# Performance work log

Measured on AMD Instinct MI355X. Metric: run time of the kernel, lower is better.

Reference implementation:

```python
import jax, jax.numpy as jnp
import numpy as np

EPSILON = 100.0
NITER = 10


def setup_inputs() -> dict:
    key = jax.random.key(0)
    k1, k2 = jax.random.split(key)
    n, d = 1024, 256
    output = jax.random.normal(k1, (n, d), dtype=jnp.float32)
    target = jax.random.normal(k2, (n, d), dtype=jnp.float32)
    return {"output": output, "target": target}


def _sinkhorn_loss_primal(x, y, epsilon, niter):
    n = x.shape[0]
    # L1 pairwise cost: C[i, j] = sum_k |x[i, k] - y[j, k]|   -> [n, n]
    C = jnp.sum(jnp.abs(x[:, None, :] - y[None, :, :]), axis=-1)
    log_mu = jnp.log(jnp.full((n,), 1.0 / n, dtype=x.dtype))
    log_nu = log_mu

    def M(u, v):
        # (-c_ij + u_i + v_j) / epsilon
        return (-C + u[:, None] + v[None, :]) / epsilon

    def lse_rows(A):
        # matches torch: log(sum(exp(A), axis=1) + 1e-6) (unstabilized on purpose)
        return jnp.log(jnp.sum(jnp.exp(A), axis=1) + 1e-6)

    def body(carry, _):
        u, v, done = carry
        u_new = epsilon * (log_mu - lse_rows(M(u, v))) + u
        v_new = epsilon * (log_nu - lse_rows(M(u_new, v).T)) + v
        err = jnp.sum(jnp.abs(u_new - u))
        # early exit emulation: once err < 0.1 after a step, freeze duals
        u_out = jnp.where(done, u, u_new)
        v_out = jnp.where(done, v, v_new)
        done_out = jnp.logical_or(done, err < 0.1)
        return (u_out, v_out, done_out), None

    u0 = jnp.zeros((n,), dtype=x.dtype)
    v0 = jnp.zeros((n,), dtype=x.dtype)
    (u, v, _), _ = jax.lax.scan(body, (u0, v0, jnp.array(False)), None, length=niter)

    Gamma = jnp.exp(M(u, v))
    return jnp.sum(Gamma * C)


def reference(output, target):
    # normalized=False path of FeatureOptimalLoss.forward
    return _sinkhorn_loss_primal(output, target, EPSILON, NITER)
```

## Files before the change

kernel.cpp:

```cpp
#include <hip/hip_runtime.h>
#include <stdint.h>

#define N 1024
#define DD 256
#define EPS 100.0f
#define INV_EPS 0.01f
#define LOG_MU -6.93147180559945f

__device__ __forceinline__ float waveReduceSum(float s) {
#pragma unroll
  for (int m = 1; m <= 32; m <<= 1) s += __shfl_xor(s, m);
  return s;
}

__device__ __forceinline__ uint64_t rload64(const uint64_t* p) {
  return __hip_atomic_load(p, __ATOMIC_RELAXED, __HIP_MEMORY_SCOPE_AGENT);
}
__device__ __forceinline__ void rstore64(uint64_t* p, uint64_t x) {
  __hip_atomic_store(p, x, __ATOMIC_RELAXED, __HIP_MEMORY_SCOPE_AGENT);
}
__device__ __forceinline__ uint64_t packtag(uint32_t tag, float val) {
  return ((uint64_t)tag << 32) | (uint64_t)__float_as_uint(val);
}

__device__ __forceinline__ void stage_exp(const uint64_t* __restrict__ src,
                                          uint32_t want, float* sB, int t) {
  const int base = t * 4;
  for (;;) {
    const uint64_t a0 = rload64(src + base + 0);
    const uint64_t a1 = rload64(src + base + 1);
    const uint64_t a2 = rload64(src + base + 2);
    const uint64_t a3 = rload64(src + base + 3);
    if ((uint32_t)(a0 >> 32) == want && (uint32_t)(a1 >> 32) == want &&
        (uint32_t)(a2 >> 32) == want && (uint32_t)(a3 >> 32) == want) {
      sB[base + 0] = expf(__uint_as_float((uint32_t)a0) * INV_EPS);
      sB[base + 1] = expf(__uint_as_float((uint32_t)a1) * INV_EPS);
      sB[base + 2] = expf(__uint_as_float((uint32_t)a2) * INV_EPS);
      sB[base + 3] = expf(__uint_as_float((uint32_t)a3) * INV_EPS);
      return;
    }
    __builtin_amdgcn_s_sleep(1);
  }
}

#define NTAGS 6160

__global__ __launch_bounds__(256) void cmat_kernel(
    const float* __restrict__ x, const float* __restrict__ y,
    float* __restrict__ Km, float* __restrict__ KTm,
    uint64_t* __restrict__ tags) {
  __shared__ float xs[64][68];
  __shared__ float ys[32][68];
  const int t = threadIdx.x;
  const int bj = blockIdx.x;
  const int bi = blockIdx.y;
  if (bi == 0 && bj == 0) {
    for (int z = t; z < NTAGS; z += 256) tags[z] = 0;
  }
  const int tx = t & 15;
  const int ty = t >> 4;
  float acc[4][2] = {};
  const float* xg = x + (size_t)(bi * 64) * DD;
  const float* yg = y + (size_t)(bj * 32) * DD;
  const int c0 = tx * 2, c1 = tx * 2 + 1;
  const int yswz = ((c0 >> 3) & 1) << 2;

  for (int kc = 0; kc < DD; kc += 64) {
    __syncthreads();
#pragma unroll
    for (int it = 0; it < 4; ++it) {
      const int l = it * 256 + t;
      const int row = l >> 4, kq = l & 15;
      const float4 g =
          *reinterpret_cast<const float4*>(xg + row * DD + kc + kq * 4);
      *reinterpret_cast<float4*>(&xs[row][kq * 4]) = g;
    }
#pragma unroll
    for (int it = 0; it < 2; ++it) {
      const int l = it * 256 + t;
      const int row = l >> 4, kq = l & 15;
      const float4 g =
          *reinterpret_cast<const float4*>(yg + row * DD + kc + kq * 4);
      const int col = (kq * 4) ^ (((row >> 3) & 1) << 2);
      *reinterpret_cast<float4*>(&ys[row][col]) = g;
    }
    __syncthreads();
#pragma unroll 2
    for (int kk = 0; kk < 64; kk += 4) {
      float4 xr[4];
#pragma unroll
      for (int r = 0; r < 4; ++r)
        xr[r] = *reinterpret_cast<const float4*>(&xs[ty * 4 + r][kk]);
      const float4 ya = *reinterpret_cast<const float4*>(&ys[c0][kk ^ yswz]);
      const float4 yb = *reinterpret_cast<const float4*>(&ys[c1][kk ^ yswz]);
#pragma unroll
      for (int r = 0; r < 4; ++r) {
        acc[r][0] += fabsf(xr[r].x - ya.x) + fabsf(xr[r].y - ya.y) +
                     fabsf(xr[r].z - ya.z) + fabsf(xr[r].w - ya.w);
        acc[r][1] += fabsf(xr[r].x - yb.x) + fabsf(xr[r].y - yb.y) +
                     fabsf(xr[r].z - yb.z) + fabsf(xr[r].w - yb.w);
      }
    }
  }
  float kv[4][2];
#pragma unroll
  for (int r = 0; r < 4; ++r) {
    kv[r][0] = expf(-acc[r][0] * INV_EPS);
    kv[r][1] = expf(-acc[r][1] * INV_EPS);
  }
  const int gr0 = bi * 64 + ty * 4;
  const int gc0 = bj * 32 + c0;
#pragma unroll
  for (int r = 0; r < 4; ++r)
    *reinterpret_cast<float2*>(Km + (size_t)(gr0 + r) * N + gc0) =
        make_float2(kv[r][0], kv[r][1]);
  __syncthreads();
#pragma unroll
  for (int r = 0; r < 4; ++r) {
    xs[c0][ty * 4 + r] = kv[r][0];
    xs[c1][ty * 4 + r] = kv[r][1];
  }
  __syncthreads();
#pragma unroll
  for (int it = 0; it < 2; ++it) {
    const int l = it * 256 + t;
    const int crow = l >> 4, cq = l & 15;
    const float4 val = *reinterpret_cast<const float4*>(&xs[crow][cq * 4]);
    *reinterpret_cast<float4*>(KTm + (size_t)(bj * 32 + crow) * N + bi * 64 +
                               cq * 4) = val;
  }
}

__global__ __launch_bounds__(256, 1) void sinkhorn_coop(
    const float* __restrict__ Km, const float* __restrict__ KTm,
    uint64_t* __restrict__ U, uint64_t* __restrict__ V,
    uint64_t* __restrict__ DERR, uint64_t* __restrict__ PART,
    uint64_t* __restrict__ DONE, float* __restrict__ out) {
  const int b = blockIdx.x, t = threadIdx.x;
  const int lane = t & 63, w = t >> 6;

  if (b == 256) {
    if (w != 0) return;
    for (int it = 0; it < 9; ++it) {
      const uint32_t k = it + 1;
      float e = 0.f;
#pragma unroll
      for (int q = 0; q < 16; ++q) {
        const int idx = q * 64 + lane;
        uint64_t d;
        while ((uint32_t)((d = rload64(DERR + idx)) >> 32) != k)
          __builtin_amdgcn_s_sleep(1);
        e += __uint_as_float((uint32_t)d);
      }
      e = waveReduceSum(e);
      if (lane == 0)
        rstore64(DONE + it, ((uint64_t)k << 32) | (e < 0.1f ? 1u : 0u));
      if (__shfl(e, 0) < 0.1f) return;
    }
    return;
  }

  __shared__ float sB[N];
  __shared__ float sRed[4];
  __shared__ int sDone;
  const int i = b * 4 + w;
  const float* Krow = Km + (size_t)i * N;
  const float* Trow = KTm + (size_t)i * N;

  float ui = 0.f, vj = 0.f;
  int klast = 0;

  for (int it = 0; it < 10; ++it) {
    const uint32_t k = it + 1;
    if (it == 0) {
      *reinterpret_cast<float4*>(&sB[t * 4]) = make_float4(1.f, 1.f, 1.f, 1.f);
    } else {
      stage_exp(V + (size_t)((k - 1) & 1) * N, k - 1, sB, t);
    }
    __syncthreads();
    {
      float s = 0.f;
#pragma unroll
      for (int q = 0; q < 4; ++q) {
        const int j4 = (q * 64 + lane) * 4;
        const float4 k4 = *reinterpret_cast<const float4*>(Krow + j4);
        s += k4.x * sB[j4] + k4.y * sB[j4 + 1] + k4.z * sB[j4 + 2] +
             k4.w * sB[j4 + 3];
      }
      s = waveReduceSum(s);
      const float un =
          EPS * (LOG_MU - logf(expf(ui * INV_EPS) * s + 1e-6f)) + ui;
      const float de = fabsf(un - ui);
      ui = un;
      if (lane == 0) {
        rstore64(U + (size_t)(k & 1) * N + i, packtag(k, ui));
        if (it < 9) rstore64(DERR + i, packtag(k, de));
      }
    }
    __syncthreads();
    stage_exp(U + (size_t)(k & 1) * N, k, sB, t);
    __syncthreads();
    {
      float s = 0.f;
#pragma unroll
      for (int q = 0; q < 4; ++q) {
        const int i4 = (q * 64 + lane) * 4;
        const float4 k4 = *reinterpret_cast<const float4*>(Trow + i4);
        s += k4.x * sB[i4] + k4.y * sB[i4 + 1] + k4.z * sB[i4 + 2] +
             k4.w * sB[i4 + 3];
      }
      s = waveReduceSum(s);
      const float vn =
          EPS * (LOG_MU - logf(expf(vj * INV_EPS) * s + 1e-6f)) + vj;
      vj = vn;
      if (lane == 0) rstore64(V + (size_t)(k & 1) * N + i, packtag(k, vj));
    }
    klast = (int)k;
    if (it < 9) {
      if (t == 0) {
        uint64_t d;
        while ((uint32_t)((d = rload64(DONE + it)) >> 32) != k)
          __builtin_amdgcn_s_sleep(1);
        sDone = (int)(d & 1);
      }
      __syncthreads();
      if (sDone) break;
    }
  }
  __syncthreads();
  stage_exp(V + (size_t)(klast & 1) * N, (uint32_t)klast, sB, t);
  __syncthreads();
  {
    float sl = 0.f;
#pragma unroll
    for (int q = 0; q < 4; ++q) {
      const int j4 = (q * 64 + lane) * 4;
      const float4 k4 = *reinterpret_cast<const float4*>(Krow + j4);
      sl += (k4.x * sB[j4]) * logf(k4.x) + (k4.y * sB[j4 + 1]) * logf(k4.y) +
            (k4.z * sB[j4 + 2]) * logf(k4.z) +
            (k4.w * sB[j4 + 3]) * logf(k4.w);
    }
    sl = waveReduceSum(sl) * -EPS;
    if (lane == 0) rstore64(PART + i, packtag(1u, expf(ui * INV_EPS) * sl));
  }
  if (b == 0) {
    float acc = 0.f;
#pragma unroll
    for (int q = 0; q < 4; ++q) {
      const int idx = t * 4 + q;
      uint64_t d;
      while ((uint32_t)((d = rload64(PART + idx)) >> 32) != 1u)
        __builtin_amdgcn_s_sleep(1);
      acc += __uint_as_float((uint32_t)d);
    }
    acc = waveReduceSum(acc);
    if (lane == 0) sRed[w] = acc;
    __syncthreads();
    if (t == 0) out[0] = sRed[0] + sRed[1] + sRed[2] + sRed[3];
  }
}

extern "C" void kernel_launch(void* const* d_in, const int* in_sizes, int n_in,
                              void* d_out, int out_size, void* d_ws,
                              size_t ws_size, hipStream_t stream) {
  const float* x = (const float*)d_in[0];
  const float* y = (const float*)d_in[1];
  float* out = (float*)d_out;

  const size_t nn = (size_t)N * N;
  float* Km = (float*)d_ws;
  float* KTm = Km + nn;
  uint64_t* tags = (uint64_t*)(KTm + nn);
  uint64_t* U = tags;
  uint64_t* V = U + 2 * N;
  uint64_t* DERR = V + 2 * N;
  uint64_t* PART = DERR + N;
  uint64_t* DONE = PART + N;

  cmat_kernel<<<dim3(32, 16), 256, 0, stream>>>(x, y, Km, KTm, tags);
  sinkhorn_coop<<<257, 256, 0, stream>>>(Km, KTm, U, V, DERR, PART, DONE, out);
}
```

Before: 61.18 us.

## Enlarge cost-matrix tiles with register prefetch and fuse final loss into last v-update

```diff
diff --git a/kernel.cpp b/kernel.cpp
--- a/kernel.cpp
+++ b/kernel.cpp
@@ -50,20 +50,27 @@
     float* __restrict__ Km, float* __restrict__ KTm,
     uint64_t* __restrict__ tags) {
   __shared__ float xs[64][68];
-  __shared__ float ys[32][68];
+  __shared__ float ys[64][68];
   const int t = threadIdx.x;
   const int bj = blockIdx.x;
   const int bi = blockIdx.y;
   if (bi == 0 && bj == 0) {
     for (int z = t; z < NTAGS; z += 256) tags[z] = 0;
   }
-  const int tx = t & 15;
-  const int ty = t >> 4;
-  float acc[4][2] = {};
+  const int tx = t & 15, ty = t >> 4;
+  const int r0 = ty * 4, c0 = tx * 4;
   const float* xg = x + (size_t)(bi * 64) * DD;
-  const float* yg = y + (size_t)(bj * 32) * DD;
-  const int c0 = tx * 2, c1 = tx * 2 + 1;
-  const int yswz = ((c0 >> 3) & 1) << 2;
+  const float* yg = y + (size_t)(bj * 64) * DD;
+
+  float acc[4][4] = {};
+  float4 gx[4], gy[4];
+#pragma unroll
+  for (int it = 0; it < 4; ++it) {
+    const int l = it * 256 + t;
+    const int row = l >> 4, kq = l & 15;
+    gx[it] = *reinterpret_cast<const float4*>(xg + row * DD + kq * 4);
+    gy[it] = *reinterpret_cast<const float4*>(yg + row * DD + kq * 4);
+  }
 
   for (int kc = 0; kc < DD; kc += 64) {
     __syncthreads();
@@ -71,62 +78,63 @@
     for (int it = 0; it < 4; ++it) {
       const int l = it * 256 + t;
       const int row = l >> 4, kq = l & 15;
-      const float4 g =
-          *reinterpret_cast<const float4*>(xg + row * DD + kc + kq * 4);
-      *reinterpret_cast<float4*>(&xs[row][kq * 4]) = g;
-    }
-#pragma unroll
-    for (int it = 0; it < 2; ++it) {
-      const int l = it * 256 + t;
-      const int row = l >> 4, kq = l & 15;
-      const float4 g =
-          *reinterpret_cast<const float4*>(yg + row * DD + kc + kq * 4);
-      const int col = (kq * 4) ^ (((row >> 3) & 1) << 2);
-      *reinterpret_cast<float4*>(&ys[row][col]) = g;
-    }
-    __syncthreads();
-#pragma unroll 2
+      *reinterpret_cast<float4*>(&xs[row][kq * 4]) = gx[it];
+      *reinterpret_cast<float4*>(&ys[row][kq * 4]) = gy[it];
+    }
+    __syncthreads();
+    if (kc < DD - 64) {
+#pragma unroll
+      for (int it = 0; it < 4; ++it) {
+        const int l = it * 256 + t;
+        const int row = l >> 4, kq = l & 15;
+        gx[it] = *reinterpret_cast<const float4*>(xg + row * DD + kc + 64 +
+                                                  kq * 4);
+        gy[it] = *reinterpret_cast<const float4*>(yg + row * DD + kc + 64 +
+                                                  kq * 4);
+      }
+    }
+#pragma unroll 4
     for (int kk = 0; kk < 64; kk += 4) {
-      float4 xr[4];
-#pragma unroll
-      for (int r = 0; r < 4; ++r)
-        xr[r] = *reinterpret_cast<const float4*>(&xs[ty * 4 + r][kk]);
-      const float4 ya = *reinterpret_cast<const float4*>(&ys[c0][kk ^ yswz]);
-      const float4 yb = *reinterpret_cast<const float4*>(&ys[c1][kk ^ yswz]);
-#pragma unroll
-      for (int r = 0; r < 4; ++r) {
-        acc[r][0] += fabsf(xr[r].x - ya.x) + fabsf(xr[r].y - ya.y) +
-                     fabsf(xr[r].z - ya.z) + fabsf(xr[r].w - ya.w);
-        acc[r][1] += fabsf(xr[r].x - yb.x) + fabsf(xr[r].y - yb.y) +
-                     fabsf(xr[r].z - yb.z) + fabsf(xr[r].w - yb.w);
-      }
-    }
-  }
-  float kv[4][2];
-#pragma unroll
-  for (int r = 0; r < 4; ++r) {
-    kv[r][0] = expf(-acc[r][0] * INV_EPS);
-    kv[r][1] = expf(-acc[r][1] * INV_EPS);
-  }
-  const int gr0 = bi * 64 + ty * 4;
-  const int gc0 = bj * 32 + c0;
-#pragma unroll
-  for (int r = 0; r < 4; ++r)
-    *reinterpret_cast<float2*>(Km + (size_t)(gr0 + r) * N + gc0) =
-        make_float2(kv[r][0], kv[r][1]);
+      float4 xr[4], yc[4];
+#pragma unroll
+      for (int rr = 0; rr < 4; ++rr)
+        xr[rr] = *reinterpret_cast<const float4*>(&xs[r0 + rr][kk]);
+#pragma unroll
+      for (int cc = 0; cc < 4; ++cc)
+        yc[cc] = *reinterpret_cast<const float4*>(&ys[c0 + cc][kk]);
+#pragma unroll
+      for (int rr = 0; rr < 4; ++rr)
+#pragma unroll
+        for (int cc = 0; cc < 4; ++cc)
+          acc[rr][cc] += fabsf(xr[rr].x - yc[cc].x) +
+                         fabsf(xr[rr].y - yc[cc].y) +
+                         fabsf(xr[rr].z - yc[cc].z) +
+                         fabsf(xr[rr].w - yc[cc].w);
+    }
+  }
+  float kv[4][4];
+#pragma unroll
+  for (int rr = 0; rr < 4; ++rr)
+#pragma unroll
+    for (int cc = 0; cc < 4; ++cc) kv[rr][cc] = expf(-acc[rr][cc] * INV_EPS);
+  const int gr0 = bi * 64 + r0;
+  const int gc0 = bj * 64 + c0;
+#pragma unroll
+  for (int rr = 0; rr < 4; ++rr)
+    *reinterpret_cast<float4*>(Km + (size_t)(gr0 + rr) * N + gc0) =
+        make_float4(kv[rr][0], kv[rr][1], kv[rr][2], kv[rr][3]);
   __syncthreads();
 #pragma unroll
-  for (int r = 0; r < 4; ++r) {
-    xs[c0][ty * 4 + r] = kv[r][0];
-    xs[c1][ty * 4 + r] = kv[r][1];
-  }
+  for (int rr = 0; rr < 4; ++rr)
+#pragma unroll
+    for (int cc = 0; cc < 4; ++cc) xs[c0 + cc][r0 + rr] = kv[rr][cc];
   __syncthreads();
 #pragma unroll
-  for (int it = 0; it < 2; ++it) {
+  for (int it = 0; it < 4; ++it) {
     const int l = it * 256 + t;
     const int crow = l >> 4, cq = l & 15;
     const float4 val = *reinterpret_cast<const float4*>(&xs[crow][cq * 4]);
-    *reinterpret_cast<float4*>(KTm + (size_t)(bj * 32 + crow) * N + bi * 64 +
+    *reinterpret_cast<float4*>(KTm + (size_t)(bj * 64 + crow) * N + bi * 64 +
                                cq * 4) = val;
   }
 }
@@ -200,7 +208,7 @@
     __syncthreads();
     stage_exp(U + (size_t)(k & 1) * N, k, sB, t);
     __syncthreads();
-    {
+    if (it < 9) {
       float s = 0.f;
 #pragma unroll
       for (int q = 0; q < 4; ++q) {
@@ -210,13 +218,9 @@
              k4.w * sB[i4 + 3];
       }
       s = waveReduceSum(s);
-      const float vn =
-          EPS * (LOG_MU - logf(expf(vj * INV_EPS) * s + 1e-6f)) + vj;
-      vj = vn;
+      vj = EPS * (LOG_MU - logf(expf(vj * INV_EPS) * s + 1e-6f)) + vj;
       if (lane == 0) rstore64(V + (size_t)(k & 1) * N + i, packtag(k, vj));
-    }
-    klast = (int)k;
-    if (it < 9) {
+      klast = (int)k;
       if (t == 0) {
         uint64_t d;
         while ((uint32_t)((d = rload64(DONE + it)) >> 32) != k)
@@ -225,12 +229,28 @@
       }
       __syncthreads();
       if (sDone) break;
-    }
-  }
-  __syncthreads();
-  stage_exp(V + (size_t)(klast & 1) * N, (uint32_t)klast, sB, t);
-  __syncthreads();
-  {
+    } else {
+      float s = 0.f, sl = 0.f;
+#pragma unroll
+      for (int q = 0; q < 4; ++q) {
+        const int i4 = (q * 64 + lane) * 4;
+        const float4 k4 = *reinterpret_cast<const float4*>(Trow + i4);
+        const float p0 = k4.x * sB[i4], p1 = k4.y * sB[i4 + 1],
+                    p2 = k4.z * sB[i4 + 2], p3 = k4.w * sB[i4 + 3];
+        s += p0 + p1 + p2 + p3;
+        sl += p0 * logf(k4.x) + p1 * logf(k4.y) + p2 * logf(k4.z) +
+              p3 * logf(k4.w);
+      }
+      s = waveReduceSum(s);
+      sl = waveReduceSum(sl) * -EPS;
+      vj = EPS * (LOG_MU - logf(expf(vj * INV_EPS) * s + 1e-6f)) + vj;
+      if (lane == 0) rstore64(PART + i, packtag(1u, expf(vj * INV_EPS) * sl));
+      klast = 10;
+    }
+  }
+  if (klast < 10) {
+    stage_exp(V + (size_t)(klast & 1) * N, (uint32_t)klast, sB, t);
+    __syncthreads();
     float sl = 0.f;
 #pragma unroll
     for (int q = 0; q < 4; ++q) {
@@ -277,6 +297,6 @@
   uint64_t* PART = DERR + N;
   uint64_t* DONE = PART + N;
 
-  cmat_kernel<<<dim3(32, 16), 256, 0, stream>>>(x, y, Km, KTm, tags);
+  cmat_kernel<<<dim3(16, 16), 256, 0, stream>>>(x, y, Km, KTm, tags);
   sinkhorn_coop<<<257, 256, 0, stream>>>(Km, KTm, U, V, DERR, PART, DONE, out);
 }
```

After: 70.28 us. 1.15x slower.

## Cache K rows in LDS, publish exp-scaled duals, fuse final loss into last iteration

Applied to the files above, without the earlier changes.

```diff
diff --git a/kernel.cpp b/kernel.cpp
--- a/kernel.cpp
+++ b/kernel.cpp
@@ -23,8 +23,8 @@
   return ((uint64_t)tag << 32) | (uint64_t)__float_as_uint(val);
 }
 
-__device__ __forceinline__ void stage_exp(const uint64_t* __restrict__ src,
-                                          uint32_t want, float* sB, int t) {
+__device__ __forceinline__ void stage_cp(const uint64_t* __restrict__ src,
+                                         uint32_t want, float* sB, int t) {
   const int base = t * 4;
   for (;;) {
     const uint64_t a0 = rload64(src + base + 0);
@@ -33,10 +33,10 @@
     const uint64_t a3 = rload64(src + base + 3);
     if ((uint32_t)(a0 >> 32) == want && (uint32_t)(a1 >> 32) == want &&
         (uint32_t)(a2 >> 32) == want && (uint32_t)(a3 >> 32) == want) {
-      sB[base + 0] = expf(__uint_as_float((uint32_t)a0) * INV_EPS);
-      sB[base + 1] = expf(__uint_as_float((uint32_t)a1) * INV_EPS);
-      sB[base + 2] = expf(__uint_as_float((uint32_t)a2) * INV_EPS);
-      sB[base + 3] = expf(__uint_as_float((uint32_t)a3) * INV_EPS);
+      sB[base + 0] = __uint_as_float((uint32_t)a0);
+      sB[base + 1] = __uint_as_float((uint32_t)a1);
+      sB[base + 2] = __uint_as_float((uint32_t)a2);
+      sB[base + 3] = __uint_as_float((uint32_t)a3);
       return;
     }
     __builtin_amdgcn_s_sleep(1);
@@ -160,12 +160,25 @@
     return;
   }
 
+  __shared__ float Ksh[4][N];
+  __shared__ float Tsh[4][N];
   __shared__ float sB[N];
   __shared__ float sRed[4];
   __shared__ int sDone;
   const int i = b * 4 + w;
-  const float* Krow = Km + (size_t)i * N;
-  const float* Trow = KTm + (size_t)i * N;
+
+#pragma unroll
+  for (int q = 0; q < 4; ++q) {
+    const int idx = q * 256 + t;
+    const int rr = idx >> 8, cc = idx & 255;
+    *reinterpret_cast<float4*>(&Ksh[rr][cc * 4]) =
+        *reinterpret_cast<const float4*>(Km + (size_t)(b * 4 + rr) * N +
+                                         cc * 4);
+    *reinterpret_cast<float4*>(&Tsh[rr][cc * 4]) =
+        *reinterpret_cast<const float4*>(KTm + (size_t)(b * 4 + rr) * N +
+                                         cc * 4);
+  }
+  __syncthreads();
 
   float ui = 0.f, vj = 0.f;
   int klast = 0;
@@ -175,7 +188,7 @@
     if (it == 0) {
       *reinterpret_cast<float4*>(&sB[t * 4]) = make_float4(1.f, 1.f, 1.f, 1.f);
     } else {
-      stage_exp(V + (size_t)((k - 1) & 1) * N, k - 1, sB, t);
+      stage_cp(V + (size_t)((k - 1) & 1) * N, k - 1, sB, t);
     }
     __syncthreads();
     {
@@ -183,7 +196,7 @@
 #pragma unroll
       for (int q = 0; q < 4; ++q) {
         const int j4 = (q * 64 + lane) * 4;
-        const float4 k4 = *reinterpret_cast<const float4*>(Krow + j4);
+        const float4 k4 = *reinterpret_cast<const float4*>(&Ksh[w][j4]);
         s += k4.x * sB[j4] + k4.y * sB[j4 + 1] + k4.z * sB[j4 + 2] +
              k4.w * sB[j4 + 3];
       }
@@ -193,30 +206,27 @@
       const float de = fabsf(un - ui);
       ui = un;
       if (lane == 0) {
-        rstore64(U + (size_t)(k & 1) * N + i, packtag(k, ui));
+        rstore64(U + (size_t)(k & 1) * N + i, packtag(k, expf(ui * INV_EPS)));
         if (it < 9) rstore64(DERR + i, packtag(k, de));
       }
     }
     __syncthreads();
-    stage_exp(U + (size_t)(k & 1) * N, k, sB, t);
-    __syncthreads();
-    {
+    stage_cp(U + (size_t)(k & 1) * N, k, sB, t);
+    __syncthreads();
+    if (it < 9) {
       float s = 0.f;
 #pragma unroll
       for (int q = 0; q < 4; ++q) {
         const int i4 = (q * 64 + lane) * 4;
-        const float4 k4 = *reinterpret_cast<const float4*>(Trow + i4);
+        const float4 k4 = *reinterpret_cast<const float4*>(&Tsh[w][i4]);
         s += k4.x * sB[i4] + k4.y * sB[i4 + 1] + k4.z * sB[i4 + 2] +
              k4.w * sB[i4 + 3];
       }
       s = waveReduceSum(s);
-      const float vn =
-          EPS * (LOG_MU - logf(expf(vj * INV_EPS) * s + 1e-6f)) + vj;
-      vj = vn;
-      if (lane == 0) rstore64(V + (size_t)(k & 1) * N + i, packtag(k, vj));
-    }
-    klast = (int)k;
-    if (it < 9) {
+      vj = EPS * (LOG_MU - logf(expf(vj * INV_EPS) * s + 1e-6f)) + vj;
+      if (lane == 0)
+        rstore64(V + (size_t)(k & 1) * N + i, packtag(k, expf(vj * INV_EPS)));
+      klast = (int)k;
       if (t == 0) {
         uint64_t d;
         while ((uint32_t)((d = rload64(DONE + it)) >> 32) != k)
@@ -225,17 +235,33 @@
       }
       __syncthreads();
       if (sDone) break;
-    }
-  }
-  __syncthreads();
-  stage_exp(V + (size_t)(klast & 1) * N, (uint32_t)klast, sB, t);
-  __syncthreads();
-  {
+    } else {
+      float s = 0.f, sl = 0.f;
+#pragma unroll
+      for (int q = 0; q < 4; ++q) {
+        const int i4 = (q * 64 + lane) * 4;
+        const float4 k4 = *reinterpret_cast<const float4*>(&Tsh[w][i4]);
+        const float p0 = k4.x * sB[i4], p1 = k4.y * sB[i4 + 1],
+                    p2 = k4.z * sB[i4 + 2], p3 = k4.w * sB[i4 + 3];
+        s += p0 + p1 + p2 + p3;
+        sl += p0 * logf(k4.x) + p1 * logf(k4.y) + p2 * logf(k4.z) +
+              p3 * logf(k4.w);
+      }
+      s = waveReduceSum(s);
+      sl = waveReduceSum(sl) * -EPS;
+      vj = EPS * (LOG_MU - logf(expf(vj * INV_EPS) * s + 1e-6f)) + vj;
+      if (lane == 0) rstore64(PART + i, packtag(1u, expf(vj * INV_EPS) * sl));
+      klast = 10;
+    }
+  }
+  if (klast < 10) {
+    stage_cp(V + (size_t)(klast & 1) * N, (uint32_t)klast, sB, t);
+    __syncthreads();
     float sl = 0.f;
 #pragma unroll
     for (int q = 0; q < 4; ++q) {
       const int j4 = (q * 64 + lane) * 4;
-      const float4 k4 = *reinterpret_cast<const float4*>(Krow + j4);
+      const float4 k4 = *reinterpret_cast<const float4*>(&Ksh[w][j4]);
       sl += (k4.x * sB[j4]) * logf(k4.x) + (k4.y * sB[j4 + 1]) * logf(k4.y) +
             (k4.z * sB[j4 + 2]) * logf(k4.z) +
             (k4.w * sB[j4 + 3]) * logf(k4.w);
```

Result: slower. 64.31 us (+5.1%).

## Double-buffer cost tiles via direct global-to-LDS loads; fuse final loss into last v-step

Applied to the files above, without the earlier changes.

```diff
diff --git a/kernel.cpp b/kernel.cpp
--- a/kernel.cpp
+++ b/kernel.cpp
@@ -45,12 +45,18 @@
 
 #define NTAGS 6160
 
+typedef __attribute__((address_space(3))) uint32_t lds_u32_t;
+typedef __attribute__((address_space(1))) const uint32_t glb_u32_t;
+__device__ __forceinline__ void gload_lds16(const float* g, float* l) {
+  __builtin_amdgcn_global_load_lds((glb_u32_t*)g, (lds_u32_t*)l, 16, 0, 0);
+}
+
 __global__ __launch_bounds__(256) void cmat_kernel(
     const float* __restrict__ x, const float* __restrict__ y,
     float* __restrict__ Km, float* __restrict__ KTm,
     uint64_t* __restrict__ tags) {
-  __shared__ float xs[64][68];
-  __shared__ float ys[32][68];
+  __shared__ float xsA[64 * 64], xsB[64 * 64];
+  __shared__ float ysA[32 * 64], ysB[32 * 64];
   const int t = threadIdx.x;
   const int bj = blockIdx.x;
   const int bi = blockIdx.y;
@@ -59,40 +65,43 @@
   }
   const int tx = t & 15;
   const int ty = t >> 4;
-  float acc[4][2] = {};
+  const int c0 = tx * 2, c1 = c0 + 1;
+  const int xsw = (ty & 7) << 2;
+  const int ysw = ((tx >> 1) & 7) << 2;
   const float* xg = x + (size_t)(bi * 64) * DD;
   const float* yg = y + (size_t)(bj * 32) * DD;
-  const int c0 = tx * 2, c1 = tx * 2 + 1;
-  const int yswz = ((c0 >> 3) & 1) << 2;
-
-  for (int kc = 0; kc < DD; kc += 64) {
-    __syncthreads();
-#pragma unroll
-    for (int it = 0; it < 4; ++it) {
-      const int l = it * 256 + t;
-      const int row = l >> 4, kq = l & 15;
-      const float4 g =
-          *reinterpret_cast<const float4*>(xg + row * DD + kc + kq * 4);
-      *reinterpret_cast<float4*>(&xs[row][kq * 4]) = g;
-    }
-#pragma unroll
-    for (int it = 0; it < 2; ++it) {
-      const int l = it * 256 + t;
-      const int row = l >> 4, kq = l & 15;
-      const float4 g =
-          *reinterpret_cast<const float4*>(yg + row * DD + kc + kq * 4);
-      const int col = (kq * 4) ^ (((row >> 3) & 1) << 2);
-      *reinterpret_cast<float4*>(&ys[row][col]) = g;
-    }
-    __syncthreads();
+
+  float acc[4][2] = {};
+
+  auto issue = [&](float* xs, float* ys, int kc) {
+#pragma unroll
+    for (int q = 0; q < 4; ++q) {
+      const int s = q * 256 + t;
+      const int row = s >> 4, c16 = s & 15;
+      const int g16 = c16 ^ ((row >> 2) & 7);
+      gload_lds16(xg + (size_t)row * DD + kc + g16 * 4, xs + s * 4);
+    }
+#pragma unroll
+    for (int q = 0; q < 2; ++q) {
+      const int s = q * 256 + t;
+      const int row = s >> 4, c16 = s & 15;
+      const int g16 = c16 ^ ((row >> 2) & 7);
+      gload_lds16(yg + (size_t)row * DD + kc + g16 * 4, ys + s * 4);
+    }
+  };
+
+  auto compute = [&](const float* xs, const float* ys) {
 #pragma unroll 2
     for (int kk = 0; kk < 64; kk += 4) {
       float4 xr[4];
 #pragma unroll
       for (int r = 0; r < 4; ++r)
-        xr[r] = *reinterpret_cast<const float4*>(&xs[ty * 4 + r][kk]);
-      const float4 ya = *reinterpret_cast<const float4*>(&ys[c0][kk ^ yswz]);
-      const float4 yb = *reinterpret_cast<const float4*>(&ys[c1][kk ^ yswz]);
+        xr[r] = *reinterpret_cast<const float4*>(
+            &xs[(ty * 4 + r) * 64 + (kk ^ xsw)]);
+      const float4 ya =
+          *reinterpret_cast<const float4*>(&ys[c0 * 64 + (kk ^ ysw)]);
+      const float4 yb =
+          *reinterpret_cast<const float4*>(&ys[c1 * 64 + (kk ^ ysw)]);
 #pragma unroll
       for (int r = 0; r < 4; ++r) {
         acc[r][0] += fabsf(xr[r].x - ya.x) + fabsf(xr[r].y - ya.y) +
@@ -101,7 +110,21 @@
                      fabsf(xr[r].z - yb.z) + fabsf(xr[r].w - yb.w);
       }
     }
-  }
+  };
+
+  issue(xsA, ysA, 0);
+  __syncthreads();
+  issue(xsB, ysB, 64);
+  compute(xsA, ysA);
+  __syncthreads();
+  issue(xsA, ysA, 128);
+  compute(xsB, ysB);
+  __syncthreads();
+  issue(xsB, ysB, 192);
+  compute(xsA, ysA);
+  __syncthreads();
+  compute(xsB, ysB);
+
   float kv[4][2];
 #pragma unroll
   for (int r = 0; r < 4; ++r) {
@@ -114,18 +137,20 @@
   for (int r = 0; r < 4; ++r)
     *reinterpret_cast<float2*>(Km + (size_t)(gr0 + r) * N + gc0) =
         make_float2(kv[r][0], kv[r][1]);
-  __syncthreads();
+  float* trans = xsA;
+  const int tsw = (tx >> 1) & 7;
 #pragma unroll
   for (int r = 0; r < 4; ++r) {
-    xs[c0][ty * 4 + r] = kv[r][0];
-    xs[c1][ty * 4 + r] = kv[r][1];
+    trans[c0 * 64 + ((ty ^ tsw) << 2) + r] = kv[r][0];
+    trans[c1 * 64 + ((ty ^ tsw) << 2) + r] = kv[r][1];
   }
   __syncthreads();
 #pragma unroll
   for (int it = 0; it < 2; ++it) {
     const int l = it * 256 + t;
     const int crow = l >> 4, cq = l & 15;
-    const float4 val = *reinterpret_cast<const float4*>(&xs[crow][cq * 4]);
+    const float4 val = *reinterpret_cast<const float4*>(
+        &trans[crow * 64 + ((cq ^ ((crow >> 2) & 7)) << 2)]);
     *reinterpret_cast<float4*>(KTm + (size_t)(bj * 32 + crow) * N + bi * 64 +
                                cq * 4) = val;
   }
@@ -200,7 +225,7 @@
     __syncthreads();
     stage_exp(U + (size_t)(k & 1) * N, k, sB, t);
     __syncthreads();
-    {
+    if (it < 9) {
       float s = 0.f;
 #pragma unroll
       for (int q = 0; q < 4; ++q) {
@@ -210,13 +235,9 @@
              k4.w * sB[i4 + 3];
       }
       s = waveReduceSum(s);
-      const float vn =
-          EPS * (LOG_MU - logf(expf(vj * INV_EPS) * s + 1e-6f)) + vj;
-      vj = vn;
+      vj = EPS * (LOG_MU - logf(expf(vj * INV_EPS) * s + 1e-6f)) + vj;
       if (lane == 0) rstore64(V + (size_t)(k & 1) * N + i, packtag(k, vj));
-    }
-    klast = (int)k;
-    if (it < 9) {
+      klast = (int)k;
       if (t == 0) {
         uint64_t d;
         while ((uint32_t)((d = rload64(DONE + it)) >> 32) != k)
@@ -225,12 +246,28 @@
       }
       __syncthreads();
       if (sDone) break;
-    }
-  }
-  __syncthreads();
-  stage_exp(V + (size_t)(klast & 1) * N, (uint32_t)klast, sB, t);
-  __syncthreads();
-  {
+    } else {
+      float s = 0.f, sl = 0.f;
+#pragma unroll
+      for (int q = 0; q < 4; ++q) {
+        const int i4 = (q * 64 + lane) * 4;
+        const float4 k4 = *reinterpret_cast<const float4*>(Trow + i4);
+        const float p0 = k4.x * sB[i4], p1 = k4.y * sB[i4 + 1],
+                    p2 = k4.z * sB[i4 + 2], p3 = k4.w * sB[i4 + 3];
+        s += p0 + p1 + p2 + p3;
+        sl += p0 * logf(k4.x) + p1 * logf(k4.y) + p2 * logf(k4.z) +
+              p3 * logf(k4.w);
+      }
+      s = waveReduceSum(s);
+      sl = waveReduceSum(sl) * -EPS;
+      vj = EPS * (LOG_MU - logf(expf(vj * INV_EPS) * s + 1e-6f)) + vj;
+      if (lane == 0) rstore64(PART + i, packtag(1u, expf(vj * INV_EPS) * sl));
+      klast = 10;
+    }
+  }
+  if (klast < 10) {
+    stage_exp(V + (size_t)(klast & 1) * N, (uint32_t)klast, sB, t);
+    __syncthreads();
     float sl = 0.f;
 #pragma unroll
     for (int q = 0; q < 4; ++q) {
```

New measurement: 59.00 us. 1.04x faster.
